# Kernel tuning notes

Hardware: AMD Instinct MI355X
Metric: run time of the kernel (lower is better)

The kernel has to match this reference:

```python
import jax, jax.numpy as jnp
import numpy as np

B, S, D, H = 4, 2048, 1024, 16
HD = D // H  # 64


def setup_inputs() -> dict:
    key = jax.random.key(0)
    ks = jax.random.split(key, 9)
    s = 1.0 / np.sqrt(D)
    return {
        "x": jax.random.normal(ks[0], (B, S, D), dtype=jnp.float32),
        "Wq": jax.random.normal(ks[1], (D, D), dtype=jnp.float32) * s,
        "bq": jax.random.normal(ks[2], (D,), dtype=jnp.float32) * 0.01,
        "Wk": jax.random.normal(ks[3], (D, D), dtype=jnp.float32) * s,
        "bk": jax.random.normal(ks[4], (D,), dtype=jnp.float32) * 0.01,
        "Wv": jax.random.normal(ks[5], (D, D), dtype=jnp.float32) * s,
        "bv": jax.random.normal(ks[6], (D,), dtype=jnp.float32) * 0.01,
        "Wo": jax.random.normal(ks[7], (D, D), dtype=jnp.float32) * s,
        "bo": jax.random.normal(ks[8], (D,), dtype=jnp.float32) * 0.01,
    }


def reference(x, Wq, bq, Wk, bk, Wv, bv, Wo, bo):
    b, s, _ = x.shape
    # projections -> [b, h, s, hd]
    def proj(W, bias):
        return (x @ W.T + bias).reshape(b, s, H, HD).transpose(0, 2, 1, 3)
    q, k, v = proj(Wq, bq), proj(Wk, bk), proj(Wv, bv)
    # NOTE: source multiplies by sqrt(head_dim)**0.5 = head_dim**0.25 (quirk kept)
    scale = jnp.asarray(HD, dtype=x.dtype) ** 0.25
    scores = jnp.einsum("bhqd,bhkd->bhqk", q, k) * scale
    causal = jnp.tril(jnp.ones((s, s), dtype=bool))
    scores = jnp.where(causal, scores, -jnp.inf)
    attn = jax.nn.softmax(scores, axis=-1)  # dropout p=0 (eval) -> identity
    out = jnp.einsum("bhqk,bhkd->bhqd", attn, v)
    out = out.transpose(0, 2, 1, 3).reshape(b, s, D)
    return out @ Wo.T + bo
```

## Files before the change

### kernel.cpp

```cpp
#include <hip/hip_runtime.h>
#include <hip/hip_fp16.h>


typedef unsigned short u16;
typedef unsigned int u32;
typedef _Float16 half8 __attribute__((ext_vector_type(8)));
typedef float f32x4 __attribute__((ext_vector_type(4)));
typedef unsigned short ushort8 __attribute__((ext_vector_type(8)));
typedef unsigned short us4 __attribute__((ext_vector_type(4)));
typedef unsigned int u32x2 __attribute__((ext_vector_type(2)));

#define SCL2 4.0816663172343815f
#define SWZ(r) ((((r) ^ ((r) >> 3))) & 7)

__device__ __forceinline__ u16 f2h(float f) {
  return __half_as_ushort(__float2half(f));
}

__device__ __forceinline__ us4 pack4(float a, float b, float c, float d) {
  u32x2 t;
  t[0] = __builtin_bit_cast(u32, __builtin_amdgcn_cvt_pkrtz(a, b));
  t[1] = __builtin_bit_cast(u32, __builtin_amdgcn_cvt_pkrtz(c, d));
  return __builtin_bit_cast(us4, t);
}

__device__ __forceinline__ void gload16(const void* gsrc, void* ldst) {
  typedef __attribute__((address_space(1))) const void glob_t;
  typedef __attribute__((address_space(3))) void lds_t;
  __builtin_amdgcn_global_load_lds((glob_t*)gsrc, (lds_t*)ldst, 16, 0, 0);
}

__device__ __forceinline__ f32x4 mfma_f16(half8 a, half8 b, f32x4 c) {
  return __builtin_amdgcn_mfma_f32_16x16x32_f16(a, b, c, 0, 0, 0);
}

__global__ __launch_bounds__(256) void cvt_f32_f16(const float* __restrict__ in,
                                                   u16* __restrict__ out, int n8) {
  int i = blockIdx.x * 256 + threadIdx.x;
  if (i >= n8) return;
  const float4* p = (const float4*)in + (size_t)i * 2;
  float4 a = p[0], b = p[1];
  ushort8 v;
  v[0] = f2h(a.x); v[1] = f2h(a.y); v[2] = f2h(a.z); v[3] = f2h(a.w);
  v[4] = f2h(b.x); v[5] = f2h(b.y); v[6] = f2h(b.z); v[7] = f2h(b.w);
  *(ushort8*)(out + (size_t)i * 8) = v;
}

__device__ __forceinline__ void gemm_body(const u16* __restrict__ A, const u16* __restrict__ Bw,
                                          const float* __restrict__ bias,
                                          u16* __restrict__ Ch, float* __restrict__ Cf,
                                          u16* __restrict__ Vtp, int m0, int n0) {
  __shared__ __align__(16) u16 sA[2][128 * 32];
  __shared__ __align__(16) u16 sB[2][128 * 32];
  const int tid = threadIdx.x, w = tid >> 6, l = tid & 63;
  const int wm = (w >> 1) * 64, wn = (w & 1) * 64;
  f32x4 acc[4][4] = {};
  const int srow = tid >> 2;
  const int sch = ((tid & 3) ^ ((srow >> 1) & 3)) * 8;
  const u16* Ag0 = A + (size_t)(m0 + srow) * 1024 + sch;
  const u16* Ag1 = A + (size_t)(m0 + 64 + srow) * 1024 + sch;
  const u16* Bg0 = Bw + (size_t)(n0 + srow) * 1024 + sch;
  const u16* Bg1 = Bw + (size_t)(n0 + 64 + srow) * 1024 + sch;
  auto stage = [&](int buf, int k0) {
    char* a = (char*)sA[buf] + w * 1024;
    char* b = (char*)sB[buf] + w * 1024;
    gload16(Ag0 + k0, a);
    gload16(Ag1 + k0, a + 4096);
    gload16(Bg0 + k0, b);
    gload16(Bg1 + k0, b + 4096);
  };
  stage(0, 0);
  __syncthreads();
  int cur = 0;
  const int ca = ((l >> 4) ^ (((l & 15) >> 1) & 3)) * 8;
  for (int kt = 0; kt < 32; ++kt) {
    if (kt < 31) stage(cur ^ 1, (kt + 1) * 32);
    half8 a[4], b[4];
#pragma unroll
    for (int mf = 0; mf < 4; ++mf)
      a[mf] = *(const half8*)&sA[cur][(wm + mf * 16 + (l & 15)) * 32 + ca];
#pragma unroll
    for (int nf = 0; nf < 4; ++nf)
      b[nf] = *(const half8*)&sB[cur][(wn + nf * 16 + (l & 15)) * 32 + ca];
#pragma unroll
    for (int mf = 0; mf < 4; ++mf)
#pragma unroll
      for (int nf = 0; nf < 4; ++nf)
        acc[mf][nf] = mfma_f16(a[mf], b[nf], acc[mf][nf]);
    __syncthreads();
    cur ^= 1;
  }
  if (Vtp) {
#pragma unroll
    for (int nf = 0; nf < 4; ++nf) {
      const int col = n0 + wn + nf * 16 + (l & 15);
      const float bv = bias[col];
#pragma unroll
      for (int mf = 0; mf < 4; ++mf) {
        const int row = m0 + wm + mf * 16 + (l >> 4) * 4;
        us4 v;
#pragma unroll
        for (int r = 0; r < 4; ++r) v[r] = f2h(acc[mf][nf][r] + bv);
        *(us4*)(Vtp + (size_t)((row >> 11) * 16 + (col >> 6)) * 131072 +
                (size_t)(col & 63) * 2048 + (row & 2047)) = v;
      }
    }
  } else {
#pragma unroll
    for (int nf = 0; nf < 4; ++nf) {
      const int col = n0 + wn + nf * 16 + (l & 15);
      const float bv = bias[col];
#pragma unroll
      for (int mf = 0; mf < 4; ++mf) {
#pragma unroll
        for (int r = 0; r < 4; ++r) {
          const int row = m0 + wm + mf * 16 + (l >> 4) * 4 + r;
          float v = acc[mf][nf][r] + bv;
          if (Cf) Cf[(size_t)row * 1024 + col] = v;
          else    Ch[(size_t)row * 1024 + col] = f2h(v);
        }
      }
    }
  }
}

struct QkvArgs {
  const u16* B[3];
  const float* bias[3];
  u16* C[3];
};

__global__ __launch_bounds__(256) void gemm_qkv(const u16* __restrict__ A, QkvArgs ga) {
  const int lin = blockIdx.x;
  const int wid = (lin & 7) * 192 + (lin >> 3);
  const int mblk = wid / 24;
  const int rem = wid - mblk * 24;
  const int z = rem >> 3, nblk = rem & 7;
  if (z == 2) gemm_body(A, ga.B[2], ga.bias[2], nullptr, nullptr, ga.C[2], mblk * 128, nblk * 128);
  else        gemm_body(A, ga.B[z], ga.bias[z], ga.C[z], nullptr, nullptr, mblk * 128, nblk * 128);
}

__global__ __launch_bounds__(256) void gemm_out(const u16* __restrict__ A, const u16* __restrict__ Bw,
                                                const float* __restrict__ bias, float* __restrict__ C) {
  const int lin = blockIdx.x;
  const int wid = (lin & 7) * 64 + (lin >> 3);
  const int mblk = wid >> 3, nblk = wid & 7;
  gemm_body(A, Bw, bias, nullptr, C, nullptr, mblk * 128, nblk * 128);
}

__global__ __launch_bounds__(256) void attn_fused(const u16* __restrict__ Qb, const u16* __restrict__ Kb,
                                                  const u16* __restrict__ Vt, u16* __restrict__ Ob) {
  __shared__ __align__(16) u16 k_s[2 * 64 * 64];
  __shared__ __align__(16) u16 vt_s[2 * 64 * 64];
  __shared__ __align__(16) u16 p_s[4 * 16 * 64];
  const int bid = blockIdx.x;
  const int bh = bid & 63;
  const int pj = bid >> 6;
  const int b = bh >> 4, h = bh & 15;
  const size_t baseQ = (size_t)b * 2048 * 1024 + h * 64;
  const size_t baseV = (size_t)(b * 16 + h) * 131072;
  const int tid = threadIdx.x, w = tid >> 6, l = tid & 63;
  const int g = l >> 4, qi = l & 15;
  const int q_loc = w * 16 + qi;

  const int srow = w * 8 + (l >> 3);
  const int sch0 = (l & 7) ^ SWZ(srow);
  const int sch1 = (l & 7) ^ SWZ(srow + 32);
  int koff[4], pvoff[2], voff[4][2];
#pragma unroll
  for (int nf = 0; nf < 4; ++nf) {
    const int row = nf * 16 + qi;
    koff[nf] = row * 64 + ((g ^ SWZ(row)) << 3);
#pragma unroll
    for (int ks = 0; ks < 2; ++ks)
      voff[nf][ks] = row * 64 + (((ks * 4 + g) ^ SWZ(row)) << 3);
  }
#pragma unroll
  for (int ks = 0; ks < 2; ++ks)
    pvoff[ks] = qi * 64 + (((ks * 4 + g) ^ SWZ(qi)) << 3);
  u16* pw = p_s + w * 1024;

  const u16* pK0;
  const u16* pK1;
  const u16* pV0;
  const u16* pV1;
  auto stage = [&](int buf) {
    char* kb = (char*)k_s + buf * 8192;
    char* vb = (char*)vt_s + buf * 8192;
    gload16(pK0, kb + w * 1024);
    gload16(pK1, kb + 4096 + w * 1024);
    gload16(pV0, vb + w * 1024);
    gload16(pV1, vb + 4096 + w * 1024);
    pK0 += 65536; pK1 += 65536; pV0 += 64; pV1 += 64;
  };

  int cur = 0;
  for (int half = 0; half < 2; ++half) {
    const int qt = half ? (31 - pj) : pj;
    const int q0 = qt * 64;
    const int q_glob = q0 + q_loc;

    half8 qf0, qf1;
    {
      const u16* qp = Qb + baseQ + (size_t)q_glob * 1024 + g * 8;
      qf0 = *(const half8*)(qp);
      qf1 = *(const half8*)(qp + 32);
    }
    pK0 = Kb + baseQ + (size_t)srow * 1024 + sch0 * 8;
    pK1 = Kb + baseQ + (size_t)(srow + 32) * 1024 + sch1 * 8;
    pV0 = Vt + baseV + (size_t)srow * 2048 + sch0 * 8;
    pV1 = Vt + baseV + (size_t)(srow + 32) * 2048 + sch1 * 8;

    f32x4 s[4], o[4] = {};
    float m_r = -INFINITY, l_r = 0.f;

    stage(cur);
    __syncthreads();

    for (int kt = 0; kt <= qt; ++kt) {
      if (kt < qt) stage(cur ^ 1);
      const u16* kbuf = k_s + cur * 4096;
      const u16* vbuf = vt_s + cur * 4096;
#pragma unroll
      for (int nf = 0; nf < 4; ++nf) {
        half8 k0 = *(const half8*)(kbuf + koff[nf]);
        half8 k1 = *(const half8*)(kbuf + (koff[nf] ^ 32));
        f32x4 acc = {};
        acc = mfma_f16(k0, qf0, acc);
        acc = mfma_f16(k1, qf1, acc);
        s[nf] = acc * SCL2;
      }
      if (kt == qt) {
#pragma unroll
        for (int nf = 0; nf < 4; ++nf) {
          const int kb = nf * 16 + g * 4;
#pragma unroll
          for (int r = 0; r < 4; ++r)
            if (kb + r > q_loc) s[nf][r] = -INFINITY;
        }
      }
      float t = fmaxf(fmaxf(fmaxf(s[0][0], s[0][1]), s[0][2]),
                      fmaxf(fmaxf(s[0][3], s[1][0]), s[1][1]));
      t = fmaxf(t, fmaxf(fmaxf(s[1][2], s[1][3]), s[2][0]));
      t = fmaxf(t, fmaxf(fmaxf(s[2][1], s[2][2]), s[2][3]));
      t = fmaxf(t, fmaxf(fmaxf(s[3][0], s[3][1]), s[3][2]));
      t = fmaxf(t, s[3][3]);
      t = fmaxf(t, __shfl_xor(t, 16));
      t = fmaxf(t, __shfl_xor(t, 32));
      if (!__all(t <= m_r + 8.f)) {
        const float mn = fmaxf(m_r, t);
        const float al = __builtin_amdgcn_exp2f(m_r - mn);
        l_r *= al;
#pragma unroll
        for (int nf = 0; nf < 4; ++nf) o[nf] *= al;
        m_r = mn;
      }
      float rs = 0.f;
#pragma unroll
      for (int nf = 0; nf < 4; ++nf) {
#pragma unroll
        for (int r = 0; r < 4; ++r) {
          const float p = __builtin_amdgcn_exp2f(s[nf][r] - m_r);
          s[nf][r] = p;
          rs += p;
        }
      }
      rs += __shfl_xor(rs, 16);
      rs += __shfl_xor(rs, 32);
      l_r += rs;
#pragma unroll
      for (int nf = 0; nf < 4; ++nf) {
        const int c = nf * 2 + (g >> 1);
        *(us4*)(pw + qi * 64 + ((c ^ SWZ(qi)) << 3) + (g & 1) * 4) =
            pack4(s[nf][0], s[nf][1], s[nf][2], s[nf][3]);
      }
#pragma unroll
      for (int ks = 0; ks < 2; ++ks) {
        half8 pf = *(const half8*)(pw + pvoff[ks]);
#pragma unroll
        for (int nf = 0; nf < 4; ++nf) {
          half8 vf = *(const half8*)(vbuf + voff[nf][ks]);
          o[nf] = mfma_f16(vf, pf, o[nf]);
        }
      }
      __syncthreads();
      cur ^= 1;
    }
    const float inv = 1.f / l_r;
    u16* op = Ob + (size_t)(b * 2048 + q_glob) * 1024 + h * 64 + g * 4;
#pragma unroll
    for (int nf = 0; nf < 4; ++nf)
      *(us4*)(op + nf * 16) =
          pack4(o[nf][0] * inv, o[nf][1] * inv, o[nf][2] * inv, o[nf][3] * inv);
  }
}

extern "C" void kernel_launch(void* const* d_in, const int* in_sizes, int n_in,
                              void* d_out, int out_size, void* d_ws, size_t ws_size,
                              hipStream_t stream) {
  (void)in_sizes; (void)n_in; (void)out_size; (void)ws_size;
  const float* x  = (const float*)d_in[0];
  const float* Wq = (const float*)d_in[1];
  const float* bq = (const float*)d_in[2];
  const float* Wk = (const float*)d_in[3];
  const float* bk = (const float*)d_in[4];
  const float* Wv = (const float*)d_in[5];
  const float* bv = (const float*)d_in[6];
  const float* Wo = (const float*)d_in[7];
  const float* bo = (const float*)d_in[8];

  u16* xb = (u16*)d_ws;
  u16* wq = xb + (size_t)8192 * 1024;
  u16* wk = wq + 1024 * 1024;
  u16* wv = wk + 1024 * 1024;
  u16* wo = wv + 1024 * 1024;
  u16* Qb = wo + 1024 * 1024;
  u16* Kb = Qb + (size_t)8192 * 1024;
  u16* Vt = Kb + (size_t)8192 * 1024;
  u16* Ab = xb;

  cvt_f32_f16<<<4096, 256, 0, stream>>>(x, xb, 1048576);
  cvt_f32_f16<<<512, 256, 0, stream>>>(Wq, wq, 131072);
  cvt_f32_f16<<<512, 256, 0, stream>>>(Wk, wk, 131072);
  cvt_f32_f16<<<512, 256, 0, stream>>>(Wv, wv, 131072);
  cvt_f32_f16<<<512, 256, 0, stream>>>(Wo, wo, 131072);

  QkvArgs ga;
  ga.B[0] = wq; ga.B[1] = wk; ga.B[2] = wv;
  ga.bias[0] = bq; ga.bias[1] = bk; ga.bias[2] = bv;
  ga.C[0] = Qb; ga.C[1] = Kb; ga.C[2] = Vt;
  gemm_qkv<<<1536, 256, 0, stream>>>(xb, ga);

  attn_fused<<<1024, 256, 0, stream>>>(Qb, Kb, Vt, Ab);

  gemm_out<<<512, 256, 0, stream>>>(Ab, wo, bo, (float*)d_out);
}
```

Before: 297.8 us.

## Enlarge GEMM tiles to 256x128x64 with 8 waves, XOR swizzle and setprio

The shared projection GEMM body moves from 128x128 tiles with K-step 32 and 4 waves to 256x128 tiles with K-step 64 and 8 waves per 512-thread block. Each wave now owns 128x32 of the output. The LDS layout uses an 8-way XOR swizzle, and the MFMA bursts are wrapped in s_setprio. The aim is more reuse per global load, half as many K-loop barriers, and fewer LDS bank conflicts. The cost is fewer blocks: 768 for QKV and 256 for the output GEMM. With double buffering the kernel needs 96KB of LDS, which can limit occupancy and load balance across CUs.

```diff
diff --git a/kernel.cpp b/kernel.cpp
--- a/kernel.cpp
+++ b/kernel.cpp
@@ -50,54 +50,91 @@
                                           const float* __restrict__ bias,
                                           u16* __restrict__ Ch, float* __restrict__ Cf,
                                           u16* __restrict__ Vtp, int m0, int n0) {
-  __shared__ __align__(16) u16 sA[2][128 * 32];
-  __shared__ __align__(16) u16 sB[2][128 * 32];
+  __shared__ __align__(16) u16 sA[2][256 * 64];
+  __shared__ __align__(16) u16 sB[2][128 * 64];
   const int tid = threadIdx.x, w = tid >> 6, l = tid & 63;
-  const int wm = (w >> 1) * 64, wn = (w & 1) * 64;
-  f32x4 acc[4][4] = {};
-  const int srow = tid >> 2;
-  const int sch = ((tid & 3) ^ ((srow >> 1) & 3)) * 8;
-  const u16* Ag0 = A + (size_t)(m0 + srow) * 1024 + sch;
-  const u16* Ag1 = A + (size_t)(m0 + 64 + srow) * 1024 + sch;
-  const u16* Bg0 = Bw + (size_t)(n0 + srow) * 1024 + sch;
-  const u16* Bg1 = Bw + (size_t)(n0 + 64 + srow) * 1024 + sch;
+  const int g = l >> 4, fr = l & 15;
+  const int wm = (w >> 2) * 128, wn = (w & 3) * 32;
+  f32x4 acc[8][2] = {};
+  const int srow8 = w * 8 + (l >> 3);
+  size_t aoff[4], boff[2];
+#pragma unroll
+  for (int i = 0; i < 4; ++i) {
+    const int row = i * 64 + srow8;
+    aoff[i] = (size_t)(m0 + row) * 1024 + ((l & 7) ^ SWZ(row)) * 8;
+  }
+#pragma unroll
+  for (int i = 0; i < 2; ++i) {
+    const int row = i * 64 + srow8;
+    boff[i] = (size_t)(n0 + row) * 1024 + ((l & 7) ^ SWZ(row)) * 8;
+  }
+  const int ldst = w * 1024 + l * 16;
   auto stage = [&](int buf, int k0) {
-    char* a = (char*)sA[buf] + w * 1024;
-    char* b = (char*)sB[buf] + w * 1024;
-    gload16(Ag0 + k0, a);
-    gload16(Ag1 + k0, a + 4096);
-    gload16(Bg0 + k0, b);
-    gload16(Bg1 + k0, b + 4096);
+    char* ab = (char*)sA[buf];
+    char* bb = (char*)sB[buf];
+#pragma unroll
+    for (int i = 0; i < 4; ++i) gload16(A + aoff[i] + k0, ab + i * 8192 + ldst);
+#pragma unroll
+    for (int i = 0; i < 2; ++i) gload16(Bw + boff[i] + k0, bb + i * 8192 + ldst);
   };
+  int aofr[8][2], bofr[2][2];
+#pragma unroll
+  for (int mf = 0; mf < 8; ++mf) {
+    const int row = wm + mf * 16 + fr;
+#pragma unroll
+    for (int kk = 0; kk < 2; ++kk)
+      aofr[mf][kk] = row * 64 + (((kk * 4 + g) ^ SWZ(row)) << 3);
+  }
+#pragma unroll
+  for (int nf = 0; nf < 2; ++nf) {
+    const int row = wn + nf * 16 + fr;
+#pragma unroll
+    for (int kk = 0; kk < 2; ++kk)
+      bofr[nf][kk] = row * 64 + (((kk * 4 + g) ^ SWZ(row)) << 3);
+  }
+
   stage(0, 0);
   __syncthreads();
-  int cur = 0;
-  const int ca = ((l >> 4) ^ (((l & 15) >> 1) & 3)) * 8;
-  for (int kt = 0; kt < 32; ++kt) {
-    if (kt < 31) stage(cur ^ 1, (kt + 1) * 32);
-    half8 a[4], b[4];
-#pragma unroll
-    for (int mf = 0; mf < 4; ++mf)
-      a[mf] = *(const half8*)&sA[cur][(wm + mf * 16 + (l & 15)) * 32 + ca];
-#pragma unroll
-    for (int nf = 0; nf < 4; ++nf)
-      b[nf] = *(const half8*)&sB[cur][(wn + nf * 16 + (l & 15)) * 32 + ca];
-#pragma unroll
-    for (int mf = 0; mf < 4; ++mf)
-#pragma unroll
-      for (int nf = 0; nf < 4; ++nf)
-        acc[mf][nf] = mfma_f16(a[mf], b[nf], acc[mf][nf]);
+  for (int t = 0; t < 16; ++t) {
+    const int cur = t & 1;
+    if (t < 15) stage(cur ^ 1, (t + 1) * 64);
+    const u16* sa = sA[cur];
+    const u16* sb = sB[cur];
+    half8 bf[2][2];
+#pragma unroll
+    for (int nf = 0; nf < 2; ++nf)
+#pragma unroll
+      for (int kk = 0; kk < 2; ++kk)
+        bf[nf][kk] = *(const half8*)&sb[bofr[nf][kk]];
+#pragma unroll
+    for (int mh = 0; mh < 2; ++mh) {
+      half8 af[4][2];
+#pragma unroll
+      for (int mq = 0; mq < 4; ++mq)
+#pragma unroll
+        for (int kk = 0; kk < 2; ++kk)
+          af[mq][kk] = *(const half8*)&sa[aofr[mh * 4 + mq][kk]];
+      __builtin_amdgcn_s_setprio(1);
+#pragma unroll
+      for (int mq = 0; mq < 4; ++mq)
+#pragma unroll
+        for (int nf = 0; nf < 2; ++nf)
+#pragma unroll
+          for (int kk = 0; kk < 2; ++kk)
+            acc[mh * 4 + mq][nf] = mfma_f16(af[mq][kk], bf[nf][kk], acc[mh * 4 + mq][nf]);
+      __builtin_amdgcn_s_setprio(0);
+    }
     __syncthreads();
-    cur ^= 1;
-  }
+  }
+
   if (Vtp) {
 #pragma unroll
-    for (int nf = 0; nf < 4; ++nf) {
-      const int col = n0 + wn + nf * 16 + (l & 15);
+    for (int nf = 0; nf < 2; ++nf) {
+      const int col = n0 + wn + nf * 16 + fr;
       const float bv = bias[col];
 #pragma unroll
-      for (int mf = 0; mf < 4; ++mf) {
-        const int row = m0 + wm + mf * 16 + (l >> 4) * 4;
+      for (int mf = 0; mf < 8; ++mf) {
+        const int row = m0 + wm + mf * 16 + g * 4;
         us4 v;
 #pragma unroll
         for (int r = 0; r < 4; ++r) v[r] = f2h(acc[mf][nf][r] + bv);
@@ -107,14 +144,14 @@
     }
   } else {
 #pragma unroll
-    for (int nf = 0; nf < 4; ++nf) {
-      const int col = n0 + wn + nf * 16 + (l & 15);
+    for (int nf = 0; nf < 2; ++nf) {
+      const int col = n0 + wn + nf * 16 + fr;
       const float bv = bias[col];
 #pragma unroll
-      for (int mf = 0; mf < 4; ++mf) {
+      for (int mf = 0; mf < 8; ++mf) {
 #pragma unroll
         for (int r = 0; r < 4; ++r) {
-          const int row = m0 + wm + mf * 16 + (l >> 4) * 4 + r;
+          const int row = m0 + wm + mf * 16 + g * 4 + r;
           float v = acc[mf][nf][r] + bv;
           if (Cf) Cf[(size_t)row * 1024 + col] = v;
           else    Ch[(size_t)row * 1024 + col] = f2h(v);
@@ -130,22 +167,22 @@
   u16* C[3];
 };
 
-__global__ __launch_bounds__(256) void gemm_qkv(const u16* __restrict__ A, QkvArgs ga) {
+__global__ __launch_bounds__(512, 2) void gemm_qkv(const u16* __restrict__ A, QkvArgs ga) {
   const int lin = blockIdx.x;
-  const int wid = (lin & 7) * 192 + (lin >> 3);
+  const int wid = (lin & 7) * 96 + (lin >> 3);
   const int mblk = wid / 24;
   const int rem = wid - mblk * 24;
   const int z = rem >> 3, nblk = rem & 7;
-  if (z == 2) gemm_body(A, ga.B[2], ga.bias[2], nullptr, nullptr, ga.C[2], mblk * 128, nblk * 128);
-  else        gemm_body(A, ga.B[z], ga.bias[z], ga.C[z], nullptr, nullptr, mblk * 128, nblk * 128);
-}
-
-__global__ __launch_bounds__(256) void gemm_out(const u16* __restrict__ A, const u16* __restrict__ Bw,
-                                                const float* __restrict__ bias, float* __restrict__ C) {
+  if (z == 2) gemm_body(A, ga.B[2], ga.bias[2], nullptr, nullptr, ga.C[2], mblk * 256, nblk * 128);
+  else        gemm_body(A, ga.B[z], ga.bias[z], ga.C[z], nullptr, nullptr, mblk * 256, nblk * 128);
+}
+
+__global__ __launch_bounds__(512, 2) void gemm_out(const u16* __restrict__ A, const u16* __restrict__ Bw,
+                                                   const float* __restrict__ bias, float* __restrict__ C) {
   const int lin = blockIdx.x;
-  const int wid = (lin & 7) * 64 + (lin >> 3);
+  const int wid = (lin & 7) * 32 + (lin >> 3);
   const int mblk = wid >> 3, nblk = wid & 7;
-  gemm_body(A, Bw, bias, nullptr, C, nullptr, mblk * 128, nblk * 128);
+  gemm_body(A, Bw, bias, nullptr, C, nullptr, mblk * 256, nblk * 128);
 }
 
 __global__ __launch_bounds__(256) void attn_fused(const u16* __restrict__ Qb, const u16* __restrict__ Kb,
@@ -329,9 +366,9 @@
   ga.B[0] = wq; ga.B[1] = wk; ga.B[2] = wv;
   ga.bias[0] = bq; ga.bias[1] = bk; ga.bias[2] = bv;
   ga.C[0] = Qb; ga.C[1] = Kb; ga.C[2] = Vt;
-  gemm_qkv<<<1536, 256, 0, stream>>>(xb, ga);
+  gemm_qkv<<<768, 512, 0, stream>>>(xb, ga);
 
   attn_fused<<<1024, 256, 0, stream>>>(Qb, Kb, Vt, Ab);
 
-  gemm_out<<<512, 256, 0, stream>>>(Ab, wo, bo, (float*)d_out);
-}
+  gemm_out<<<256, 512, 0, stream>>>(Ab, wo, bo, (float*)d_out);
+}
```

After: 294.2 us. About the same (-1.2%).
